# Kernel optimization log

Hardware: AMD Instinct MI355X
Metric: run time of the kernel (lower is better)

## Reference

```python
import jax, jax.numpy as jnp
import numpy as np

NUM_NODES = 50000
NUM_FEATS = 64
NUM_HEADS = 2
NUM_EDGES = 800000


def setup_inputs() -> dict:
    key = jax.random.key(0)
    k1, k2, k3 = jax.random.split(key, 3)
    x = jax.random.normal(k1, (NUM_NODES, NUM_FEATS), dtype=jnp.float32)
    # qk_lin: Linear(num_feats, 2*num_feats*num_heads)
    lim = 1.0 / np.sqrt(NUM_FEATS)
    W_qk = jax.random.uniform(k2, (NUM_FEATS, 2 * NUM_HEADS * NUM_FEATS),
                              dtype=jnp.float32, minval=-lim, maxval=lim)
    b_qk = jnp.zeros((2 * NUM_HEADS * NUM_FEATS,), dtype=jnp.float32)
    edge_index = jax.random.randint(k3, (2, NUM_EDGES), 0, NUM_NODES, dtype=jnp.int32)
    return {"x": x, "W_qk": W_qk, "b_qk": b_qk, "edge_index": edge_index}


def reference(x, W_qk, b_qk, edge_index):
    """Edge-restricted multi-head QK attention with sparse softmax over
    each row's outgoing edges, averaged over heads. Returns per-edge
    attention values [E] (sparse COO values; indices == edge_index)."""
    N, F = x.shape
    H = W_qk.shape[1] // (2 * F)
    # qk: [N, 2*H*F] -> [N, H, 2, F]; q/k split matches einops rearranges
    qk = (x @ W_qk + b_qk).reshape(N, H, 2, F)
    q = qk[:, :, 0, :]  # [N, H, F]
    k = qk[:, :, 1, :]  # [N, H, F]
    row, col = edge_index[0], edge_index[1]
    # per-edge per-head scores: q[row] . k[col]  -> [E, H]
    s = jnp.einsum('ehf,ehf->eh', q[row], k[col])
    # sparse softmax over dim=2 (columns) == segment softmax grouped by row
    m = jax.ops.segment_max(s, row, num_segments=N)      # [N, H]
    ex = jnp.exp(s - m[row])                             # [E, H]
    denom = jax.ops.segment_sum(ex, row, num_segments=N)  # [N, H]
    p = ex / denom[row]                                  # [E, H]
    # torch.sparse.sum over heads / num_heads == mean over heads
    return jnp.mean(p, axis=1)  # [E]
```

## Files before the change

kernel.cpp:

```cpp
#include <hip/hip_runtime.h>
#include <hip/hip_bf16.h>


#define NFEAT 64
#define NCOL  256

typedef __attribute__((ext_vector_type(8))) short bf16x8;
typedef __attribute__((ext_vector_type(4))) float f32x4;

__device__ __forceinline__ unsigned short f2bf(float f) {
    union { __hip_bfloat16 h; unsigned short u; } cv;
    cv.h = __float2bfloat16(f);
    return cv.u;
}

__global__ __launch_bounds__(256) void prep_wt(const float* __restrict__ W,
                                               unsigned short* __restrict__ Wt) {
    const int k = blockIdx.x;
    const int c = threadIdx.x;
    Wt[(size_t)c * 64 + k] = f2bf(W[(size_t)k * 256 + c]);
}

__global__ __launch_bounds__(64) void gemm_qk_mfma(
    const float* __restrict__ x, const unsigned short* __restrict__ Wt,
    const float* __restrict__ b,
    unsigned short* __restrict__ qo, unsigned short* __restrict__ ko,
    float* __restrict__ den, int N)
{
    const int lane = threadIdx.x;
    const int l15  = lane & 15;
    const int quad = lane >> 4;
    const int base = blockIdx.x * 32;

    const int t = blockIdx.x * 64 + lane;
    if (t < 2 * N) den[t] = 0.f;

    bf16x8 afrag[2][2];
#pragma unroll
    for (int s = 0; s < 2; ++s) {
        int m = base + s * 16 + l15;
        if (m >= N) m = N - 1;
        const float* xp = x + (size_t)m * NFEAT + quad * 8;
#pragma unroll
        for (int ks = 0; ks < 2; ++ks) {
            float4 a0 = *(const float4*)(xp + ks * 32);
            float4 a1 = *(const float4*)(xp + ks * 32 + 4);
            bf16x8 f;
            f[0] = f2bf(a0.x); f[1] = f2bf(a0.y); f[2] = f2bf(a0.z); f[3] = f2bf(a0.w);
            f[4] = f2bf(a1.x); f[5] = f2bf(a1.y); f[6] = f2bf(a1.z); f[7] = f2bf(a1.w);
            afrag[s][ks] = f;
        }
    }

#pragma unroll 4
    for (int ct = 0; ct < 16; ++ct) {
        const int c = ct * 16 + l15;
        bf16x8 b0 = *(const bf16x8*)(Wt + (size_t)c * 64 + quad * 8);
        bf16x8 b1 = *(const bf16x8*)(Wt + (size_t)c * 64 + 32 + quad * 8);
        const float bias = b[c];
        const int h   = c >> 7;
        const int isk = (c >> 6) & 1;
        const int f0  = c & 63;
        unsigned short* dst = isk ? ko : qo;
#pragma unroll
        for (int s = 0; s < 2; ++s) {
            f32x4 acc = {0.f, 0.f, 0.f, 0.f};
            acc = __builtin_amdgcn_mfma_f32_16x16x32_bf16(afrag[s][0], b0, acc, 0, 0, 0);
            acc = __builtin_amdgcn_mfma_f32_16x16x32_bf16(afrag[s][1], b1, acc, 0, 0, 0);
#pragma unroll
            for (int r = 0; r < 4; ++r) {
                const int m = base + s * 16 + quad * 4 + r;
                if (m < N)
                    dst[(size_t)m * 128 + h * 64 + f0] = f2bf(acc[r] + bias);
            }
        }
    }
}

__device__ __forceinline__ float dot_bf16x2(unsigned a, unsigned b) {
    float alo = __uint_as_float(a << 16), ahi = __uint_as_float(a & 0xFFFF0000u);
    float blo = __uint_as_float(b << 16), bhi = __uint_as_float(b & 0xFFFF0000u);
    return alo * blo + ahi * bhi;
}

__global__ __launch_bounds__(256) void edge_scores_exp(
    const unsigned short* __restrict__ q, const unsigned short* __restrict__ k,
    const int* __restrict__ ei, float* __restrict__ ex_out,
    float* __restrict__ denom, int E)
{
    const int g    = (int)((blockIdx.x * 256 + threadIdx.x) >> 4);
    const int lane = threadIdx.x & 15;
    if (g >= E) return;

    const int row = ei[g];
    const int col = ei[E + g];

    const uint4* qp = (const uint4*)(q + (size_t)row * 128);
    const uint4* kp = (const uint4*)(k + (size_t)col * 128);
    uint4 qa = qp[lane];
    uint4 ka = kp[lane];

    float p = dot_bf16x2(qa.x, ka.x) + dot_bf16x2(qa.y, ka.y)
            + dot_bf16x2(qa.z, ka.z) + dot_bf16x2(qa.w, ka.w);

    p += __shfl_xor(p, 1);
    p += __shfl_xor(p, 2);
    p += __shfl_xor(p, 4);

    if ((lane & 7) == 0) {
        const int h  = lane >> 3;
        const float e = __expf(p);
        ex_out[(size_t)g * 2 + h] = e;
        atomicAdd(&denom[(size_t)row * 2 + h], e);
    }
}

__global__ __launch_bounds__(256) void edge_out_k(
    const int* __restrict__ ei, const float* __restrict__ ex,
    const float* __restrict__ denom, float* __restrict__ out, int E)
{
    const int e = blockIdx.x * 256 + threadIdx.x;
    if (e >= E) return;
    const int row = ei[e];
    const float2 exv = *(const float2*)&ex[(size_t)e * 2];
    const float2 dv  = *(const float2*)&denom[(size_t)row * 2];
    out[e] = 0.5f * (exv.x / dv.x + exv.y / dv.y);
}

extern "C" void kernel_launch(void* const* d_in, const int* in_sizes, int n_in,
                              void* d_out, int out_size, void* d_ws, size_t ws_size,
                              hipStream_t stream)
{
    const float* x   = (const float*)d_in[0];
    const float* W   = (const float*)d_in[1];
    const float* b   = (const float*)d_in[2];
    const int*   ei  = (const int*)d_in[3];
    float*       out = (float*)d_out;

    const int N = in_sizes[0] / NFEAT;
    const int E = in_sizes[3] / 2;

    char* ws = (char*)d_ws;
    size_t off = 0;
    auto alloc = [&](size_t bytes) { void* p = ws + off; off += (bytes + 255) & ~(size_t)255; return p; };
    unsigned short* q_ws  = (unsigned short*)alloc((size_t)N * 128 * 2);
    unsigned short* k_ws  = (unsigned short*)alloc((size_t)N * 128 * 2);
    float*          ex_ws = (float*)alloc((size_t)E * 2 * sizeof(float));
    float*          den_ws= (float*)alloc((size_t)N * 2 * sizeof(float));
    unsigned short* wt_ws = (unsigned short*)alloc((size_t)NCOL * NFEAT * 2);
    (void)ws_size;

    prep_wt<<<NFEAT, NCOL, 0, stream>>>(W, wt_ws);
    gemm_qk_mfma<<<(N + 31) / 32, 64, 0, stream>>>(x, wt_ws, b, q_ws, k_ws, den_ws, N);
    edge_scores_exp<<<((size_t)E * 16 + 255) / 256, 256, 0, stream>>>(q_ws, k_ws, ei, ex_ws, den_ws, E);
    edge_out_k<<<(E + 255) / 256, 256, 0, stream>>>(ei, ex_ws, den_ws, out, E);
}
```

Before: 155.7 us.

## Stage W in LDS for the GEMM and batch four edges per lane group

```diff
diff --git a/kernel.cpp b/kernel.cpp
--- a/kernel.cpp
+++ b/kernel.cpp
@@ -21,19 +21,31 @@
     Wt[(size_t)c * 64 + k] = f2bf(W[(size_t)k * 256 + c]);
 }
 
-__global__ __launch_bounds__(64) void gemm_qk_mfma(
+__global__ __launch_bounds__(256) void gemm_qk_mfma(
     const float* __restrict__ x, const unsigned short* __restrict__ Wt,
     const float* __restrict__ b,
     unsigned short* __restrict__ qo, unsigned short* __restrict__ ko,
     float* __restrict__ den, int N)
 {
-    const int lane = threadIdx.x;
+    __shared__ unsigned short WtL[NCOL * NFEAT];
+    __shared__ float bL[NCOL];
+    const int tid = threadIdx.x;
+
+    for (int i = tid; i < NCOL * NFEAT / 2; i += 256)
+        ((unsigned*)WtL)[i] = ((const unsigned*)Wt)[i];
+    bL[tid] = b[tid];
+
+    const int t = blockIdx.x * 256 + tid;
+    if (t < 2 * N) den[t] = 0.f;
+
+    const int lane = tid & 63;
+    const int wv   = tid >> 6;
     const int l15  = lane & 15;
     const int quad = lane >> 4;
-    const int base = blockIdx.x * 32;
+    const int base = blockIdx.x * 128 + wv * 32;
+    __syncthreads();
 
-    const int t = blockIdx.x * 64 + lane;
-    if (t < 2 * N) den[t] = 0.f;
+    if (base >= N) return;
 
     bf16x8 afrag[2][2];
 #pragma unroll
@@ -55,9 +67,9 @@
 #pragma unroll 4
     for (int ct = 0; ct < 16; ++ct) {
         const int c = ct * 16 + l15;
-        bf16x8 b0 = *(const bf16x8*)(Wt + (size_t)c * 64 + quad * 8);
-        bf16x8 b1 = *(const bf16x8*)(Wt + (size_t)c * 64 + 32 + quad * 8);
-        const float bias = b[c];
+        bf16x8 b0 = *(const bf16x8*)(WtL + (size_t)c * 64 + quad * 8);
+        bf16x8 b1 = *(const bf16x8*)(WtL + (size_t)c * 64 + 32 + quad * 8);
+        const float bias = bL[c];
         const int h   = c >> 7;
         const int isk = (c >> 6) & 1;
         const int f0  = c & 63;
@@ -88,30 +100,41 @@
     const int* __restrict__ ei, float* __restrict__ ex_out,
     float* __restrict__ denom, int E)
 {
-    const int g    = (int)((blockIdx.x * 256 + threadIdx.x) >> 4);
+    const int grp  = (int)((blockIdx.x * 256 + threadIdx.x) >> 4);
     const int lane = threadIdx.x & 15;
-    if (g >= E) return;
+    const int g0   = grp * 4;
+    if (g0 >= E) return;
 
-    const int row = ei[g];
-    const int col = ei[E + g];
+    int v = 0;
+    if (lane < 4)      v = ei[g0 + lane];
+    else if (lane < 8) v = ei[E + g0 + (lane - 4)];
+    int rows[4], cols[4];
+#pragma unroll
+    for (int i = 0; i < 4; ++i) {
+        rows[i] = __shfl(v, i, 16);
+        cols[i] = __shfl(v, 4 + i, 16);
+    }
 
-    const uint4* qp = (const uint4*)(q + (size_t)row * 128);
-    const uint4* kp = (const uint4*)(k + (size_t)col * 128);
-    uint4 qa = qp[lane];
-    uint4 ka = kp[lane];
+    uint4 qa[4], ka[4];
+#pragma unroll
+    for (int i = 0; i < 4; ++i) {
+        qa[i] = ((const uint4*)(q + (size_t)rows[i] * 128))[lane];
+        ka[i] = ((const uint4*)(k + (size_t)cols[i] * 128))[lane];
+    }
 
-    float p = dot_bf16x2(qa.x, ka.x) + dot_bf16x2(qa.y, ka.y)
-            + dot_bf16x2(qa.z, ka.z) + dot_bf16x2(qa.w, ka.w);
-
-    p += __shfl_xor(p, 1);
-    p += __shfl_xor(p, 2);
-    p += __shfl_xor(p, 4);
-
-    if ((lane & 7) == 0) {
-        const int h  = lane >> 3;
-        const float e = __expf(p);
-        ex_out[(size_t)g * 2 + h] = e;
-        atomicAdd(&denom[(size_t)row * 2 + h], e);
+#pragma unroll
+    for (int i = 0; i < 4; ++i) {
+        float p = dot_bf16x2(qa[i].x, ka[i].x) + dot_bf16x2(qa[i].y, ka[i].y)
+                + dot_bf16x2(qa[i].z, ka[i].z) + dot_bf16x2(qa[i].w, ka[i].w);
+        p += __shfl_xor(p, 1);
+        p += __shfl_xor(p, 2);
+        p += __shfl_xor(p, 4);
+        if ((lane & 7) == 0) {
+            const int h  = lane >> 3;
+            const float e = __expf(p);
+            ex_out[(size_t)(g0 + i) * 2 + h] = e;
+            atomicAdd(&denom[(size_t)rows[i] * 2 + h], e);
+        }
     }
 }
 
@@ -151,7 +174,7 @@
     (void)ws_size;
 
     prep_wt<<<NFEAT, NCOL, 0, stream>>>(W, wt_ws);
-    gemm_qk_mfma<<<(N + 31) / 32, 64, 0, stream>>>(x, wt_ws, b, q_ws, k_ws, den_ws, N);
-    edge_scores_exp<<<((size_t)E * 16 + 255) / 256, 256, 0, stream>>>(q_ws, k_ws, ei, ex_ws, den_ws, E);
+    gemm_qk_mfma<<<(N + 127) / 128, 256, 0, stream>>>(x, wt_ws, b, q_ws, k_ws, den_ws, N);
+    edge_scores_exp<<<((size_t)(E + 3) / 4 * 16 + 255) / 256, 256, 0, stream>>>(q_ws, k_ws, ei, ex_ws, den_ws, E);
     edge_out_k<<<(E + 255) / 256, 256, 0, stream>>>(ei, ex_ws, den_ws, out, E);
 }
```

Result: faster. 143.5 us (-7.9%).
